# Performance work log

Hardware: AMD Instinct MI355X
Metric: run time of the kernel (lower is better)

The kernel has to match this reference:

```python
import jax, jax.numpy as jnp
import numpy as np

B, L, D = 8, 4096, 1024   # batch, max words, sent_dim
S, SENT_LEN = 255, 16     # sentences per sample, words per sentence (255*16=4080)
START_BOUND = 1           # leading zero-pad region, as in the torch module


def setup_inputs() -> dict:
    key = jax.random.key(0)
    k1, k2, k3, k4 = jax.random.split(key, 4)
    words_emb = jax.random.normal(k1, (B, L, D), jnp.float32)
    sents_emb = jax.random.normal(k2, (B, S, D), jnp.float32)
    # nn.Linear(2D, D): weight [D, 2D], bias [D]
    W1_w = jax.random.normal(k3, (D, 2 * D), jnp.float32) / np.sqrt(2 * D)
    W1_b = jax.random.normal(k4, (D,), jnp.float32) * 0.01
    # sentence-index-per-word map; -1 marks the zero-padded regions
    sm = -np.ones((B, L), np.int32)
    idx = np.repeat(np.arange(S, dtype=np.int32), SENT_LEN)  # [S*SENT_LEN]
    sm[:, START_BOUND:START_BOUND + S * SENT_LEN] = idx
    sent_map = jnp.asarray(sm)
    return {"words_emb": words_emb, "sents_emb": sents_emb,
            "W1_w": W1_w, "W1_b": W1_b, "sent_map": sent_map}


def reference(words_emb, sents_emb, W1_w, W1_b, sent_map):
    # Expand sentence embeddings to word positions via gather; zero outside spans.
    valid = sent_map >= 0                                    # [B, L]
    safe_idx = jnp.clip(sent_map, 0)                         # [B, L]
    gathered = jnp.take_along_axis(sents_emb, safe_idx[..., None], axis=1)  # [B, L, D]
    sents_state_flat = jnp.where(valid[..., None], gathered, 0.0)
    # concat word + sentence features, then Linear + ReLU
    x = jnp.concatenate([words_emb, sents_state_flat], axis=-1)  # [B, L, 2D]
    return jax.nn.relu(jnp.einsum('ble,de->bld', x, W1_w) + W1_b)
```

## Files before the change

kernel.cpp:

```cpp
#include <hip/hip_runtime.h>
#include <stdint.h>

constexpr int kB = 8;
constexpr int kL = 4096;
constexpr int kD = 1024;
constexpr int kS = 255;
constexpr int kM = kB * kL;
constexpr int kK = 2 * kD;
constexpr int kN = kD;

typedef __bf16 bf16x8 __attribute__((ext_vector_type(8)));
typedef float  f32x4  __attribute__((ext_vector_type(4)));

constexpr size_t WS_WORDS = 0;
constexpr size_t WS_SENTS = WS_WORDS + (size_t)kM * kD * 2;
constexpr size_t WS_W     = WS_SENTS + (size_t)kB * kS * kD * 2;
constexpr size_t WS_ZP    = WS_W + (size_t)kN * kK * 2;
constexpr size_t WS_NEED  = WS_ZP + 3072;

__device__ __forceinline__ uint32_t pk_bf16x2(float a, float b) {
    uint32_t ua = __float_as_uint(a) + 0x8000u;
    uint32_t ub = __float_as_uint(b) + 0x8000u;
    return __builtin_amdgcn_perm(ub, ua, 0x07060302u);
}

__device__ __forceinline__ void async16(const void* g, void* l) {
    __builtin_amdgcn_global_load_lds(
        (const __attribute__((address_space(1))) uint32_t*)g,
        (__attribute__((address_space(3))) uint32_t*)l, 16, 0, 0);
}

#define WAITVM(n)  asm volatile("s_waitcnt vmcnt(" #n ")" ::: "memory")
#define WAITLGKM0  asm volatile("s_waitcnt lgkmcnt(0)" ::: "memory")

__device__ __forceinline__ void blockbar() {
    __builtin_amdgcn_sched_barrier(0);
    __builtin_amdgcn_s_barrier();
    __builtin_amdgcn_sched_barrier(0);
}

__global__ __launch_bounds__(256)
void cvt_prepass2(const float4* __restrict__ words, const float4* __restrict__ sents,
                  const float4* __restrict__ W,
                  uint4* __restrict__ wordsB, uint4* __restrict__ sentsB,
                  uint4* __restrict__ WB, uint32_t* __restrict__ zp)
{
    constexpr size_t NW8 = (size_t)kM * kD / 8;
    constexpr size_t NS8 = (size_t)kB * kS * kD / 8;
    constexpr size_t NB8 = (size_t)kN * kK / 8;
    constexpr size_t NT8 = NW8 + NS8 + NB8;
    if (blockIdx.x == 0) {
        for (int t = threadIdx.x; t < 768; t += 256) zp[t] = 0u;
    }
    const size_t stride = (size_t)gridDim.x * blockDim.x;
    for (size_t i = (size_t)blockIdx.x * blockDim.x + threadIdx.x; i < NT8; i += stride) {
        const float4* src; uint4* dst; size_t j;
        if (i < NW8)            { src = words; dst = wordsB; j = i; }
        else if (i < NW8 + NS8) { src = sents; dst = sentsB; j = i - NW8; }
        else                    { src = W;     dst = WB;     j = i - NW8 - NS8; }
        float4 a  = src[2 * j];
        float4 b2 = src[2 * j + 1];
        uint4 o;
        o.x = pk_bf16x2(a.x,  a.y);
        o.y = pk_bf16x2(a.z,  a.w);
        o.z = pk_bf16x2(b2.x, b2.y);
        o.w = pk_bf16x2(b2.z, b2.w);
        dst[j] = o;
    }
}

__global__ __launch_bounds__(512, 2)
void wsib_gemm_v5(const uint8_t* __restrict__ wordsB,
                  const uint8_t* __restrict__ sentsB,
                  const uint8_t* __restrict__ WB,
                  const float*   __restrict__ bias,
                  const int*     __restrict__ smap,
                  const uint8_t* __restrict__ zp,
                  float* __restrict__ out)
{
    __shared__ uint8_t lds[4][2][16384];

    const int tid  = threadIdx.x;
    const int w    = tid >> 6;
    const int lane = tid & 63;
    const int nT = blockIdx.x;
    const int mT = blockIdx.y;

    const int wm = (w >> 2) * 128;
    const int wn = (w & 3) * 64;
    const int fr = lane & 15, quad = lane >> 4;

    float bv[4];
    #pragma unroll
    for (int ni = 0; ni < 4; ++ni) bv[ni] = bias[nT * 256 + wn + ni * 16 + fr];

    const int lrow = lane >> 2;
    const int ch   = (lane & 3) * 16;
    const int rloc0 = w * 32 + lrow, rloc1 = rloc0 + 16;
    const int gA0 = mT * 256 + rloc0, gA1 = mT * 256 + rloc1;
    const int bIdx = gA0 >> 12;
    const uint8_t* aw0 = wordsB + (size_t)gA0 * 2048 + ch;
    const uint8_t* aw1 = wordsB + (size_t)gA1 * 2048 + ch;
    const int s0 = smap[gA0], s1 = smap[gA1];
    const uint8_t* as0 = (s0 >= 0) ? sentsB + (size_t)(bIdx * kS + s0) * 2048 + ch : zp + ch;
    const uint8_t* as1 = (s1 >= 0) ? sentsB + (size_t)(bIdx * kS + s1) * 2048 + ch : zp + ch;
    const uint8_t* pB0 = WB + (size_t)(nT * 256 + rloc0) * 4096 + ch;
    const uint8_t* pB1 = WB + (size_t)(nT * 256 + rloc1) * 4096 + ch;

    auto stage = [&](int buf, int t) {
        uint8_t* A  = (uint8_t*)lds[buf][0];
        uint8_t* Bb = (uint8_t*)lds[buf][1];
        const uint8_t* a0 = (t < 32) ? aw0 + t * 64 : as0 + (t - 32) * 64;
        const uint8_t* a1 = (t < 32) ? aw1 + t * 64 : as1 + (t - 32) * 64;
        async16(a0, A + w * 2048);
        async16(a1, A + w * 2048 + 1024);
        async16(pB0 + t * 64, Bb + w * 2048);
        async16(pB1 + t * 64, Bb + w * 2048 + 1024);
    };

    const int offA = (wm + fr) * 64 + quad * 16;
    const int offB = (wn + fr) * 64 + quad * 16;

    f32x4 acc[8][4];
    #pragma unroll
    for (int i = 0; i < 8; ++i)
        #pragma unroll
        for (int j = 0; j < 4; ++j) acc[i][j] = (f32x4){0.f, 0.f, 0.f, 0.f};

    stage(0, 0);
    stage(1, 1);
    stage(2, 2);
    WAITVM(8);
    blockbar();

    bf16x8 af[4], bfA[4], bfB[4];
    #pragma unroll
    for (int mi = 0; mi < 4; ++mi)
        af[mi] = *(const bf16x8*)((uint8_t*)lds[0][0] + offA + mi * 1024);
    #pragma unroll
    for (int ni = 0; ni < 4; ++ni)
        bfA[ni] = *(const bf16x8*)((uint8_t*)lds[0][1] + offB + ni * 1024);

    auto kstep = [&](int t, bf16x8 (&bfc)[4], bf16x8 (&bfn)[4]) {
        uint8_t* bufT = (uint8_t*)lds[t & 3][0];

        bf16x8 ag[4];
        #pragma unroll
        for (int mi = 0; mi < 4; ++mi)
            ag[mi] = *(const bf16x8*)(bufT + offA + (mi + 4) * 1024);
        __builtin_amdgcn_s_setprio(1);
        #pragma unroll
        for (int mi = 0; mi < 4; ++mi)
            #pragma unroll
            for (int ni = 0; ni < 4; ++ni)
                acc[mi][ni] = __builtin_amdgcn_mfma_f32_16x16x32_bf16(
                    af[mi], bfc[ni], acc[mi][ni], 0, 0, 0);
        __builtin_amdgcn_s_setprio(0);

        WAITLGKM0;
        if (t < 62) { WAITVM(4); } else { WAITVM(0); }
        blockbar();

        if (t + 3 < 64) stage((t + 3) & 3, t + 3);
        if (t + 1 < 64) {
            uint8_t* bufNA = (uint8_t*)lds[(t + 1) & 3][0];
            uint8_t* bufNB = (uint8_t*)lds[(t + 1) & 3][1];
            #pragma unroll
            for (int ni = 0; ni < 4; ++ni)
                bfn[ni] = *(const bf16x8*)(bufNB + offB + ni * 1024);
            #pragma unroll
            for (int mi = 0; mi < 4; ++mi)
                af[mi] = *(const bf16x8*)(bufNA + offA + mi * 1024);
        }
        __builtin_amdgcn_s_setprio(1);
        #pragma unroll
        for (int mi = 0; mi < 4; ++mi)
            #pragma unroll
            for (int ni = 0; ni < 4; ++ni)
                acc[mi + 4][ni] = __builtin_amdgcn_mfma_f32_16x16x32_bf16(
                    ag[mi], bfc[ni], acc[mi + 4][ni], 0, 0, 0);
        __builtin_amdgcn_s_setprio(0);
    };

    #pragma unroll 1
    for (int t2 = 0; t2 < 32; ++t2) {
        kstep(2 * t2,     bfA, bfB);
        kstep(2 * t2 + 1, bfB, bfA);
    }

    const int rowBase = mT * 256 + wm + quad * 4;
    const int colBase = nT * 256 + wn + fr;
    #pragma unroll
    for (int mi = 0; mi < 8; ++mi) {
        #pragma unroll
        for (int ni = 0; ni < 4; ++ni) {
            const int col = colBase + ni * 16;
            #pragma unroll
            for (int r = 0; r < 4; ++r) {
                const int row = rowBase + mi * 16 + r;
                out[(size_t)row * kN + col] = fmaxf(acc[mi][ni][r] + bv[ni], 0.f);
            }
        }
    }
}

#define TILE_M 128
#define TILE_N 128
#define TILE_K 32
#define LDS_STRIDE 20
__global__ __launch_bounds__(256)
void wsib_gemm_fb(const float* __restrict__ words, const float* __restrict__ sents,
                  const float* __restrict__ W, const float* __restrict__ bias,
                  const int* __restrict__ smap, float* __restrict__ out)
{
    __shared__ uint32_t Asm[TILE_M * LDS_STRIDE];
    __shared__ uint32_t Bsm[TILE_N * LDS_STRIDE];
    const int tid = threadIdx.x, nT = blockIdx.x, mT = blockIdx.y;
    const int sRow = tid >> 1, half = tid & 1;
    const int mRow = mT * TILE_M + sRow, bIdx = mRow >> 12;
    const float* wsrc = words + (size_t)mRow * kD + half * 16;
    const int sidx = smap[mRow];
    const float* ssrc = (sidx >= 0) ? sents + ((size_t)bIdx * kS + sidx) * kD + half * 16 : nullptr;
    const float* bsrc = W + (size_t)(nT * TILE_N + sRow) * kK + half * 16;
    uint32_t* adst = &Asm[sRow * LDS_STRIDE + half * 8];
    uint32_t* bdst = &Bsm[sRow * LDS_STRIDE + half * 8];
    const int lane = tid & 63, wv = tid >> 6;
    const int wm = (wv & 1) * 64, wn = (wv >> 1) * 64;
    const int fr = lane & 15, quad = lane >> 4;
    f32x4 acc[4][4];
    #pragma unroll
    for (int i = 0; i < 4; ++i)
        #pragma unroll
        for (int j = 0; j < 4; ++j) acc[i][j] = (f32x4){0.f, 0.f, 0.f, 0.f};
    float4 ra[4], rb[4];
    {
        const float4* pa = (const float4*)wsrc; const float4* pb = (const float4*)bsrc;
        #pragma unroll
        for (int i = 0; i < 4; ++i) { ra[i] = pa[i]; rb[i] = pb[i]; }
    }
    for (int k0 = 0; k0 < kK; k0 += TILE_K) {
        uint32_t pa[8], pb[8];
        #pragma unroll
        for (int i = 0; i < 4; ++i) {
            pa[2*i] = pk_bf16x2(ra[i].x, ra[i].y); pa[2*i+1] = pk_bf16x2(ra[i].z, ra[i].w);
            pb[2*i] = pk_bf16x2(rb[i].x, rb[i].y); pb[2*i+1] = pk_bf16x2(rb[i].z, rb[i].w);
        }
        __syncthreads();
        ((uint4*)adst)[0] = make_uint4(pa[0], pa[1], pa[2], pa[3]);
        ((uint4*)adst)[1] = make_uint4(pa[4], pa[5], pa[6], pa[7]);
        ((uint4*)bdst)[0] = make_uint4(pb[0], pb[1], pb[2], pb[3]);
        ((uint4*)bdst)[1] = make_uint4(pb[4], pb[5], pb[6], pb[7]);
        __syncthreads();
        const int k1 = k0 + TILE_K;
        if (k1 < kK) {
            const float* asrc = (k1 < kD) ? (wsrc + k1) : (ssrc ? (ssrc + (k1 - kD)) : nullptr);
            if (asrc) { const float4* p = (const float4*)asrc;
                #pragma unroll
                for (int i = 0; i < 4; ++i) ra[i] = p[i];
            } else {
                #pragma unroll
                for (int i = 0; i < 4; ++i) ra[i] = make_float4(0.f, 0.f, 0.f, 0.f);
            }
            const float4* p = (const float4*)(bsrc + k1);
            #pragma unroll
            for (int i = 0; i < 4; ++i) rb[i] = p[i];
        }
        bf16x8 af[4], bfv[4];
        #pragma unroll
        for (int mi = 0; mi < 4; ++mi)
            af[mi] = *(const bf16x8*)&Asm[(wm + mi * 16 + fr) * LDS_STRIDE + quad * 4];
        #pragma unroll
        for (int ni = 0; ni < 4; ++ni)
            bfv[ni] = *(const bf16x8*)&Bsm[(wn + ni * 16 + fr) * LDS_STRIDE + quad * 4];
        #pragma unroll
        for (int mi = 0; mi < 4; ++mi)
            #pragma unroll
            for (int ni = 0; ni < 4; ++ni)
                acc[mi][ni] = __builtin_amdgcn_mfma_f32_16x16x32_bf16(af[mi], bfv[ni], acc[mi][ni], 0, 0, 0);
    }
    const int rowBase = mT * TILE_M + wm, colBase = nT * TILE_N + wn;
    float bv[4];
    #pragma unroll
    for (int ni = 0; ni < 4; ++ni) bv[ni] = bias[colBase + ni * 16 + fr];
    #pragma unroll
    for (int mi = 0; mi < 4; ++mi)
        #pragma unroll
        for (int ni = 0; ni < 4; ++ni) {
            const int col = colBase + ni * 16 + fr;
            #pragma unroll
            for (int r = 0; r < 4; ++r) {
                const int row = rowBase + mi * 16 + quad * 4 + r;
                out[(size_t)row * kN + col] = fmaxf(acc[mi][ni][r] + bv[ni], 0.f);
            }
        }
}

extern "C" void kernel_launch(void* const* d_in, const int* in_sizes, int n_in,
                              void* d_out, int out_size, void* d_ws, size_t ws_size,
                              hipStream_t stream) {
    const float* words = (const float*)d_in[0];
    const float* sents = (const float*)d_in[1];
    const float* W     = (const float*)d_in[2];
    const float* bias  = (const float*)d_in[3];
    const int*   smap  = (const int*)d_in[4];
    float* out = (float*)d_out;

    if (ws_size >= WS_NEED) {
        uint8_t* ws = (uint8_t*)d_ws;
        uint4* wordsB = (uint4*)(ws + WS_WORDS);
        uint4* sentsB = (uint4*)(ws + WS_SENTS);
        uint4* WB     = (uint4*)(ws + WS_W);
        uint32_t* zp  = (uint32_t*)(ws + WS_ZP);
        cvt_prepass2<<<2048, 256, 0, stream>>>(
            (const float4*)words, (const float4*)sents, (const float4*)W,
            wordsB, sentsB, WB, zp);
        dim3 grid(kN / 256, kM / 256);
        wsib_gemm_v5<<<grid, 512, 0, stream>>>(
            (const uint8_t*)wordsB, (const uint8_t*)sentsB, (const uint8_t*)WB,
            bias, smap, (const uint8_t*)zp, out);
    } else {
        dim3 grid(kN / TILE_N, kM / TILE_M);
        wsib_gemm_fb<<<grid, 256, 0, stream>>>(words, sents, W, bias, smap, out);
    }
}
```

Before: 365.4 us.

## Restructure GEMM main loop to 2-stage BK=64 with quadrant-phased MFMA and staggered loads

Replaces the 4-deep BK=32 LDS ring with a double-buffered BK=64 scheme that uses a fragment-friendly LDS layout (16-row slabs read by lane*16). Each k-tile is split into four MFMA quadrants, with A and B global prefetches for the next tile issued between phases, guarded by many block barriers and sched_barriers. The aim is fewer pipeline iterations, conflict-free LDS reads and an interleave of loads with MFMA, a layout similar to hipBLASLt-style ping-pong. The cost is more barriers per iteration, a shallower prefetch depth that waits on vmcnt(0) every tile, and the same 128KB of LDS. Two blocks per CU remain possible.

Measured after the change: 391.8 us. 1.07x slower.

```diff
diff --git a/kernel.cpp b/kernel.cpp
--- a/kernel.cpp
+++ b/kernel.cpp
@@ -70,7 +70,7 @@
 }
 
 __global__ __launch_bounds__(512, 2)
-void wsib_gemm_v5(const uint8_t* __restrict__ wordsB,
+void wsib_gemm_v6(const uint8_t* __restrict__ wordsB,
                   const uint8_t* __restrict__ sentsB,
                   const uint8_t* __restrict__ WB,
                   const float*   __restrict__ bias,
@@ -78,7 +78,7 @@
                   const uint8_t* __restrict__ zp,
                   float* __restrict__ out)
 {
-    __shared__ uint8_t lds[4][2][16384];
+    __shared__ uint8_t lds[2][2][32768];
 
     const int tid  = threadIdx.x;
     const int w    = tid >> 6;
@@ -89,37 +89,41 @@
     const int wm = (w >> 2) * 128;
     const int wn = (w & 3) * 64;
     const int fr = lane & 15, quad = lane >> 4;
+    const int lo = lane * 16;
+    const int slabA = wm >> 4;
+    const int slabB = wn >> 4;
 
     float bv[4];
     #pragma unroll
     for (int ni = 0; ni < 4; ++ni) bv[ni] = bias[nT * 256 + wn + ni * 16 + fr];
 
-    const int lrow = lane >> 2;
-    const int ch   = (lane & 3) * 16;
-    const int rloc0 = w * 32 + lrow, rloc1 = rloc0 + 16;
-    const int gA0 = mT * 256 + rloc0, gA1 = mT * 256 + rloc1;
-    const int bIdx = gA0 >> 12;
-    const uint8_t* aw0 = wordsB + (size_t)gA0 * 2048 + ch;
-    const uint8_t* aw1 = wordsB + (size_t)gA1 * 2048 + ch;
-    const int s0 = smap[gA0], s1 = smap[gA1];
-    const uint8_t* as0 = (s0 >= 0) ? sentsB + (size_t)(bIdx * kS + s0) * 2048 + ch : zp + ch;
-    const uint8_t* as1 = (s1 >= 0) ? sentsB + (size_t)(bIdx * kS + s1) * 2048 + ch : zp + ch;
-    const uint8_t* pB0 = WB + (size_t)(nT * 256 + rloc0) * 4096 + ch;
-    const uint8_t* pB1 = WB + (size_t)(nT * 256 + rloc1) * 4096 + ch;
-
-    auto stage = [&](int buf, int t) {
-        uint8_t* A  = (uint8_t*)lds[buf][0];
-        uint8_t* Bb = (uint8_t*)lds[buf][1];
-        const uint8_t* a0 = (t < 32) ? aw0 + t * 64 : as0 + (t - 32) * 64;
-        const uint8_t* a1 = (t < 32) ? aw1 + t * 64 : as1 + (t - 32) * 64;
-        async16(a0, A + w * 2048);
-        async16(a1, A + w * 2048 + 1024);
-        async16(pB0 + t * 64, Bb + w * 2048);
-        async16(pB1 + t * 64, Bb + w * 2048 + 1024);
+    const int rb   = ((tid >> 7) << 4) + (tid & 15);
+    const int colb = ((tid >> 4) & 7) * 16;
+    const uint8_t* pAW[4]; const uint8_t* pAS[4]; const uint8_t* pB[4];
+    const int bIdx = (mT * 256) >> 12;
+    #pragma unroll
+    for (int j = 0; j < 4; ++j) {
+        const int rA = mT * 256 + rb + j * 64;
+        pAW[j] = wordsB + (size_t)rA * 2048 + colb;
+        const int s = smap[rA];
+        pAS[j] = (s >= 0) ? sentsB + (size_t)(bIdx * kS + s) * 2048 + colb : zp + colb;
+        pB[j]  = WB + (size_t)(nT * 256 + rb + j * 64) * 4096 + colb;
+    }
+
+    auto stageA = [&](int tn) {
+        uint8_t* SA = (uint8_t*)lds[tn & 1][0];
+        #pragma unroll
+        for (int j = 0; j < 4; ++j) {
+            const uint8_t* s = (tn < 16) ? pAW[j] + tn * 128 : pAS[j] + (tn - 16) * 128;
+            async16(s, SA + j * 8192 + w * 1024);
+        }
     };
-
-    const int offA = (wm + fr) * 64 + quad * 16;
-    const int offB = (wn + fr) * 64 + quad * 16;
+    auto stageB = [&](int tn) {
+        uint8_t* SB = (uint8_t*)lds[tn & 1][1];
+        #pragma unroll
+        for (int j = 0; j < 4; ++j)
+            async16(pB[j] + tn * 128, SB + j * 8192 + w * 1024);
+    };
 
     f32x4 acc[8][4];
     #pragma unroll
@@ -127,65 +131,99 @@
         #pragma unroll
         for (int j = 0; j < 4; ++j) acc[i][j] = (f32x4){0.f, 0.f, 0.f, 0.f};
 
-    stage(0, 0);
-    stage(1, 1);
-    stage(2, 2);
-    WAITVM(8);
+    stageA(0);
+    stageB(0);
+    WAITVM(0);
     blockbar();
 
-    bf16x8 af[4], bfA[4], bfB[4];
-    #pragma unroll
-    for (int mi = 0; mi < 4; ++mi)
-        af[mi] = *(const bf16x8*)((uint8_t*)lds[0][0] + offA + mi * 1024);
-    #pragma unroll
-    for (int ni = 0; ni < 4; ++ni)
-        bfA[ni] = *(const bf16x8*)((uint8_t*)lds[0][1] + offB + ni * 1024);
-
-    auto kstep = [&](int t, bf16x8 (&bfc)[4], bf16x8 (&bfn)[4]) {
-        uint8_t* bufT = (uint8_t*)lds[t & 3][0];
-
-        bf16x8 ag[4];
+    bf16x8 af[4][2], bf0[2][2], bf1[2][2];
+
+    #pragma unroll 1
+    for (int kt = 0; kt < 32; ++kt) {
+        const int P = kt & 1;
+        uint8_t* Ab = (uint8_t*)lds[P][0];
+        uint8_t* Bb = (uint8_t*)lds[P][1];
+        const int tn = kt + 1;
+
         #pragma unroll
         for (int mi = 0; mi < 4; ++mi)
-            ag[mi] = *(const bf16x8*)(bufT + offA + (mi + 4) * 1024);
+            #pragma unroll
+            for (int ks = 0; ks < 2; ++ks)
+                af[mi][ks] = *(const bf16x8*)(Ab + (slabA + mi) * 2048 + ks * 1024 + lo);
+        #pragma unroll
+        for (int ni = 0; ni < 2; ++ni)
+            #pragma unroll
+            for (int ks = 0; ks < 2; ++ks)
+                bf0[ni][ks] = *(const bf16x8*)(Bb + (slabB + ni) * 2048 + ks * 1024 + lo);
+        if (kt < 31) stageA(tn);
+        blockbar();
+        WAITLGKM0;
+        __builtin_amdgcn_sched_barrier(0);
         __builtin_amdgcn_s_setprio(1);
         #pragma unroll
+        for (int ks = 0; ks < 2; ++ks)
+            #pragma unroll
+            for (int mi = 0; mi < 4; ++mi)
+                #pragma unroll
+                for (int ni = 0; ni < 2; ++ni)
+                    acc[mi][ni] = __builtin_amdgcn_mfma_f32_16x16x32_bf16(
+                        af[mi][ks], bf0[ni][ks], acc[mi][ni], 0, 0, 0);
+        __builtin_amdgcn_s_setprio(0);
+        blockbar();
+
+        #pragma unroll
+        for (int ni = 0; ni < 2; ++ni)
+            #pragma unroll
+            for (int ks = 0; ks < 2; ++ks)
+                bf1[ni][ks] = *(const bf16x8*)(Bb + (slabB + 2 + ni) * 2048 + ks * 1024 + lo);
+        if (kt < 31) stageB(tn);
+        blockbar();
+        WAITLGKM0;
+        __builtin_amdgcn_sched_barrier(0);
+        __builtin_amdgcn_s_setprio(1);
+        #pragma unroll
+        for (int ks = 0; ks < 2; ++ks)
+            #pragma unroll
+            for (int mi = 0; mi < 4; ++mi)
+                #pragma unroll
+                for (int ni = 0; ni < 2; ++ni)
+                    acc[mi][ni + 2] = __builtin_amdgcn_mfma_f32_16x16x32_bf16(
+                        af[mi][ks], bf1[ni][ks], acc[mi][ni + 2], 0, 0, 0);
+        __builtin_amdgcn_s_setprio(0);
+        blockbar();
+
+        #pragma unroll
         for (int mi = 0; mi < 4; ++mi)
             #pragma unroll
-            for (int ni = 0; ni < 4; ++ni)
-                acc[mi][ni] = __builtin_amdgcn_mfma_f32_16x16x32_bf16(
-                    af[mi], bfc[ni], acc[mi][ni], 0, 0, 0);
+            for (int ks = 0; ks < 2; ++ks)
+                af[mi][ks] = *(const bf16x8*)(Ab + (slabA + 4 + mi) * 2048 + ks * 1024 + lo);
+        blockbar();
+        WAITLGKM0;
+        __builtin_amdgcn_sched_barrier(0);
+        __builtin_amdgcn_s_setprio(1);
+        #pragma unroll
+        for (int ks = 0; ks < 2; ++ks)
+            #pragma unroll
+            for (int mi = 0; mi < 4; ++mi)
+                #pragma unroll
+                for (int ni = 0; ni < 2; ++ni)
+                    acc[mi + 4][ni] = __builtin_amdgcn_mfma_f32_16x16x32_bf16(
+                        af[mi][ks], bf0[ni][ks], acc[mi + 4][ni], 0, 0, 0);
         __builtin_amdgcn_s_setprio(0);
-
-        WAITLGKM0;
-        if (t < 62) { WAITVM(4); } else { WAITVM(0); }
-        blockbar();
-
-        if (t + 3 < 64) stage((t + 3) & 3, t + 3);
-        if (t + 1 < 64) {
-            uint8_t* bufNA = (uint8_t*)lds[(t + 1) & 3][0];
-            uint8_t* bufNB = (uint8_t*)lds[(t + 1) & 3][1];
-            #pragma unroll
-            for (int ni = 0; ni < 4; ++ni)
-                bfn[ni] = *(const bf16x8*)(bufNB + offB + ni * 1024);
+        blockbar();
+
+        __builtin_amdgcn_s_setprio(1);
+        #pragma unroll
+        for (int ks = 0; ks < 2; ++ks)
             #pragma unroll
             for (int mi = 0; mi < 4; ++mi)
-                af[mi] = *(const bf16x8*)(bufNA + offA + mi * 1024);
-        }
-        __builtin_amdgcn_s_setprio(1);
-        #pragma unroll
-        for (int mi = 0; mi < 4; ++mi)
-            #pragma unroll
-            for (int ni = 0; ni < 4; ++ni)
-                acc[mi + 4][ni] = __builtin_amdgcn_mfma_f32_16x16x32_bf16(
-                    ag[mi], bfc[ni], acc[mi + 4][ni], 0, 0, 0);
+                #pragma unroll
+                for (int ni = 0; ni < 2; ++ni)
+                    acc[mi + 4][ni + 2] = __builtin_amdgcn_mfma_f32_16x16x32_bf16(
+                        af[mi][ks], bf1[ni][ks], acc[mi + 4][ni + 2], 0, 0, 0);
         __builtin_amdgcn_s_setprio(0);
-    };
-
-    #pragma unroll 1
-    for (int t2 = 0; t2 < 32; ++t2) {
-        kstep(2 * t2,     bfA, bfB);
-        kstep(2 * t2 + 1, bfB, bfA);
+        WAITVM(0);
+        blockbar();
     }
 
     const int rowBase = mT * 256 + wm + quad * 4;
@@ -315,7 +353,7 @@
             (const float4*)words, (const float4*)sents, (const float4*)W,
             wordsB, sentsB, WB, zp);
         dim3 grid(kN / 256, kM / 256);
-        wsib_gemm_v5<<<grid, 512, 0, stream>>>(
+        wsib_gemm_v6<<<grid, 512, 0, stream>>>(
             (const uint8_t*)wordsB, (const uint8_t*)sentsB, (const uint8_t*)WB,
             bias, smap, (const uint8_t*)zp, out);
     } else {
```
